# Kernel optimization log

Measured on AMD Instinct MI355X. Metric: run time of the kernel, lower is better.

The kernel has to match this reference:

```python
import jax, jax.numpy as jnp
from jax import lax
import numpy as np

K = 3          # kernel_size
PAD = 1        # K // 2
MAX_OFFSET = 0.1
EPS = 1e-8


def setup_inputs() -> dict:
    key = jax.random.key(0)
    k0, k1, k2 = jax.random.split(key, 3)
    B, C, H, W = 4, 64, 256, 256
    Cmid = C // 4
    x = jax.random.normal(k0, (B, C, H, W), jnp.float32)
    # offset_predictor: Conv2d(C+9, C//4, 3, pad=1) -> LeakyReLU(0.2) -> Conv2d(C//4, 2, 3, pad=1) -> Tanh
    w1 = jax.random.normal(k1, (Cmid, C + K * K, 3, 3), jnp.float32) * 0.05
    b1 = jnp.zeros((Cmid,), jnp.float32)
    w2 = jax.random.normal(k2, (2, Cmid, 3, 3), jnp.float32) * 0.05
    b2 = jnp.zeros((2,), jnp.float32)
    return {"x": x, "w1": w1, "b1": b1, "w2": w2, "b2": b2}


def _conv2d(x, w, b):
    # NCHW, OIHW, stride 1, pad 1 (SAME for 3x3)
    out = lax.conv_general_dilated(x, w, (1, 1), ((PAD, PAD), (PAD, PAD)),
                                   dimension_numbers=("NCHW", "OIHW", "NCHW"))
    return out + b[None, :, None, None]


def _local_cosine_similarity(x):
    # F.unfold with zero padding: neighbors[k] at spatial shift (di-1, dj-1), row-major k = di*K + dj
    B, C, H, W = x.shape
    xp = jnp.pad(x, ((0, 0), (0, 0), (PAD, PAD), (PAD, PAD)))
    neighbors = jnp.stack([xp[:, :, di:di + H, dj:dj + W]
                           for di in range(K) for dj in range(K)], axis=2)  # (B,C,9,H,W)
    center = x[:, :, None, :, :]                                            # (B,C,1,H,W)
    numerator = jnp.sum(neighbors * center, axis=1)                         # (B,9,H,W)
    center_norm = jnp.sqrt(jnp.sum(x * x, axis=1)) + EPS                    # (B,H,W)
    neighbor_norm = jnp.sqrt(jnp.sum(neighbors * neighbors, axis=1)) + EPS  # (B,9,H,W)
    return numerator / (center_norm[:, None] * neighbor_norm)               # (B,9,H,W)


def _grid_sample_border(x, grid):
    # bilinear, padding_mode='border', align_corners=True; grid: (B,H,W,2) with (gx,gy) in [-1,1]
    B, C, H, W = x.shape
    ix = (grid[..., 0] + 1.0) * 0.5 * (W - 1)
    iy = (grid[..., 1] + 1.0) * 0.5 * (H - 1)
    ix = jnp.clip(ix, 0.0, W - 1)
    iy = jnp.clip(iy, 0.0, H - 1)
    x0f = jnp.floor(ix); y0f = jnp.floor(iy)
    wx = ix - x0f; wy = iy - y0f
    x0 = x0f.astype(jnp.int32); y0 = y0f.astype(jnp.int32)
    x1 = jnp.minimum(x0 + 1, W - 1); y1 = jnp.minimum(y0 + 1, H - 1)

    def gather(img, yy, xx):  # img (C,H,W), yy/xx (H,W) -> (C,H,W)
        return img[:, yy, xx]

    g = jax.vmap(gather)
    v00 = g(x, y0, x0); v01 = g(x, y0, x1)
    v10 = g(x, y1, x0); v11 = g(x, y1, x1)
    wx = wx[:, None]; wy = wy[:, None]  # broadcast over channel dim
    return ((1 - wy) * ((1 - wx) * v00 + wx * v01)
            + wy * ((1 - wx) * v10 + wx * v11))


def reference(x, w1, b1, w2, b2):
    B, C, H, W = x.shape
    sim = _local_cosine_similarity(x)                       # (B,9,H,W)
    features = jnp.concatenate([x, sim], axis=1)            # (B,C+9,H,W)
    h = _conv2d(features, w1, b1)
    h = jnp.where(h >= 0, h, 0.2 * h)                       # LeakyReLU(0.2)
    offset = jnp.tanh(_conv2d(h, w2, b2)) * MAX_OFFSET      # (B,2,H,W)
    gy, gx = jnp.meshgrid(jnp.linspace(-1.0, 1.0, H),
                          jnp.linspace(-1.0, 1.0, W), indexing="ij")
    base_grid = jnp.stack([gx, gy], axis=-1)[None]          # (1,H,W,2)
    offset_grid = base_grid + jnp.transpose(offset, (0, 2, 3, 1))
    return _grid_sample_border(x, offset_grid)
```

## Files before the change

kernel.cpp:

```cpp
#include <hip/hip_runtime.h>
#include <math.h>

#define B 4
#define C 64
#define H 256
#define W 256
#define CMID 16
#define CIN 73
#define HW (H*W)
#define NW (CIN*9*CMID)
#define XS_STRIDE 260

__global__ void transpose_w1_kernel(const float* __restrict__ w1, float* __restrict__ wt) {
    int tid = blockIdx.x * blockDim.x + threadIdx.x;
    if (tid >= NW) return;
    int co = tid & (CMID - 1);
    int rest = tid >> 4;
    int ci = rest / 9;
    int k = rest - ci * 9;
    wt[tid] = w1[(co * CIN + ci) * 9 + k];
}

__device__ __forceinline__ void read_patch_lds(const float* __restrict__ xsbuf,
                                               int rl, int px, float v[3][4]) {
    const float* pb = xsbuf + rl * XS_STRIDE + px;
#pragma unroll
    for (int r = 0; r < 3; ++r) {
        float2 p0 = *(const float2*)(pb + r * XS_STRIDE);
        float2 p1 = *(const float2*)(pb + r * XS_STRIDE + 2);
        v[r][0] = p0.x; v[r][1] = p0.y; v[r][2] = p1.x; v[r][3] = p1.y;
    }
}

__global__ __launch_bounds__(256) void sim_kernel(const float* __restrict__ x,
                                                  float* __restrict__ sim) {
    __shared__ float xs[2][4 * XS_STRIDE];
    int bid = blockIdx.x;
    int b  = bid >> 7;
    int y0 = (bid & 127) << 1;
    int tid = threadIdx.x;
    int srow = tid >> 6;
    int sx4  = (tid & 63) << 2;
    int rl = tid >> 7;
    int px = (tid & 127) << 1;
    int y  = y0 + rl;

    int grow = y0 - 1 + srow;
    bool gvalid = (grow >= 0) && (grow < H);
    const float* gsrc = x + (size_t)b * C * HW + (size_t)grow * W + sx4;

    if (tid < 16) {
        int bu = tid >> 3, r = (tid >> 1) & 3, e = (tid & 1) ? 257 : 0;
        xs[bu][r * XS_STRIDE + e] = 0.f;
    }

    float dot0[9], dot1[9], nsq0[9], nsq1[9];
    float csq0 = 0.f, csq1 = 0.f;
#pragma unroll
    for (int i = 0; i < 9; ++i) { dot0[i] = dot1[i] = nsq0[i] = nsq1[i] = 0.f; }

    float4 r4 = make_float4(0.f, 0.f, 0.f, 0.f);
    if (gvalid) r4 = *(const float4*)gsrc;

    int cur = 0;
#pragma unroll 1
    for (int ci = 0; ci < C; ++ci) {
        float* dst = &xs[cur][srow * XS_STRIDE + 1 + sx4];
        dst[0] = r4.x; dst[1] = r4.y; dst[2] = r4.z; dst[3] = r4.w;
        __syncthreads();
        if (ci + 1 < C) {
            r4 = make_float4(0.f, 0.f, 0.f, 0.f);
            if (gvalid) r4 = *(const float4*)(gsrc + (size_t)(ci + 1) * HW);
        }
        float v[3][4];
        read_patch_lds(xs[cur], rl, px, v);
        float cv0 = v[1][1], cv1 = v[1][2];
        csq0 = fmaf(cv0, cv0, csq0);
        csq1 = fmaf(cv1, cv1, csq1);
#pragma unroll
        for (int kr = 0; kr < 3; ++kr)
#pragma unroll
            for (int kc = 0; kc < 3; ++kc) {
                int kk = kr * 3 + kc;
                if (kk == 4) continue;
                float n0 = v[kr][kc], n1 = v[kr][kc + 1];
                dot0[kk] = fmaf(cv0, n0, dot0[kk]);
                nsq0[kk] = fmaf(n0, n0, nsq0[kk]);
                dot1[kk] = fmaf(cv1, n1, dot1[kk]);
                nsq1[kk] = fmaf(n1, n1, nsq1[kk]);
            }
        cur ^= 1;
    }
    dot0[4] = csq0; nsq0[4] = csq0;
    dot1[4] = csq1; nsq1[4] = csq1;

    float cn0 = sqrtf(csq0) + 1e-8f;
    float cn1 = sqrtf(csq1) + 1e-8f;
    float* so = sim + (size_t)b * 9 * HW + (size_t)y * W + px;
#pragma unroll
    for (int kk = 0; kk < 9; ++kk) {
        float s0 = dot0[kk] / (cn0 * (sqrtf(nsq0[kk]) + 1e-8f));
        float s1 = dot1[kk] / (cn1 * (sqrtf(nsq1[kk]) + 1e-8f));
        *(float2*)(so + (size_t)kk * HW) = make_float2(s0, s1);
    }
}

__global__ __launch_bounds__(256) void conv1_kernel(const float* __restrict__ x,
                                                    const float* __restrict__ sim,
                                                    const float* __restrict__ wt,
                                                    const float* __restrict__ b1,
                                                    float* __restrict__ h) {
    __shared__ float lw[NW];
    __shared__ float xs[2][4 * XS_STRIDE];

    int tid = threadIdx.x;
    for (int j = tid; j < NW / 4; j += 256)
        ((float4*)lw)[j] = ((const float4*)wt)[j];

    int bid = blockIdx.x;
    int b  = bid >> 7;
    int y0 = (bid & 127) << 1;
    int srow = tid >> 6;
    int sx4  = (tid & 63) << 2;
    int rl = tid >> 7;
    int px = (tid & 127) << 1;
    int y  = y0 + rl;

    int grow = y0 - 1 + srow;
    bool gvalid = (grow >= 0) && (grow < H);
    const float* gx = x   + (size_t)b * C * HW + (size_t)grow * W + sx4;
    const float* gs = sim + (size_t)b * 9 * HW + (size_t)grow * W + sx4;

    if (tid < 16) {
        int bu = tid >> 3, r = (tid >> 1) & 3, e = (tid & 1) ? 257 : 0;
        xs[bu][r * XS_STRIDE + e] = 0.f;
    }

    float acc0[CMID], acc1[CMID];
#pragma unroll
    for (int co = 0; co < CMID; ++co) { acc0[co] = b1[co]; acc1[co] = b1[co]; }

    float4 r4 = make_float4(0.f, 0.f, 0.f, 0.f);
    if (gvalid) r4 = *(const float4*)gx;

    int cur = 0;
#pragma unroll 1
    for (int ci = 0; ci < CIN; ++ci) {
        float* dst = &xs[cur][srow * XS_STRIDE + 1 + sx4];
        dst[0] = r4.x; dst[1] = r4.y; dst[2] = r4.z; dst[3] = r4.w;
        __syncthreads();
        if (ci + 1 < CIN) {
            const float* src = (ci + 1 < C) ? (gx + (size_t)(ci + 1) * HW)
                                            : (gs + (size_t)(ci + 1 - C) * HW);
            r4 = make_float4(0.f, 0.f, 0.f, 0.f);
            if (gvalid) r4 = *(const float4*)src;
        }
        float v[3][4];
        read_patch_lds(xs[cur], rl, px, v);
        const float* wp = lw + ci * 144;
#pragma unroll
        for (int kr = 0; kr < 3; ++kr)
#pragma unroll
            for (int kc = 0; kc < 3; ++kc) {
                float a0 = v[kr][kc], a1 = v[kr][kc + 1];
                const float4* w4 = (const float4*)(wp + (kr * 3 + kc) * CMID);
#pragma unroll
                for (int q = 0; q < 4; ++q) {
                    float4 wv = w4[q];
                    acc0[4 * q + 0] = fmaf(a0, wv.x, acc0[4 * q + 0]);
                    acc0[4 * q + 1] = fmaf(a0, wv.y, acc0[4 * q + 1]);
                    acc0[4 * q + 2] = fmaf(a0, wv.z, acc0[4 * q + 2]);
                    acc0[4 * q + 3] = fmaf(a0, wv.w, acc0[4 * q + 3]);
                    acc1[4 * q + 0] = fmaf(a1, wv.x, acc1[4 * q + 0]);
                    acc1[4 * q + 1] = fmaf(a1, wv.y, acc1[4 * q + 1]);
                    acc1[4 * q + 2] = fmaf(a1, wv.z, acc1[4 * q + 2]);
                    acc1[4 * q + 3] = fmaf(a1, wv.w, acc1[4 * q + 3]);
                }
            }
        cur ^= 1;
    }

    float* ho = h + (size_t)b * CMID * HW + (size_t)y * W + px;
#pragma unroll
    for (int co = 0; co < CMID; ++co) {
        float v0 = acc0[co], v1 = acc1[co];
        v0 = v0 >= 0.f ? v0 : 0.2f * v0;
        v1 = v1 >= 0.f ? v1 : 0.2f * v1;
        *(float2*)(ho + (size_t)co * HW) = make_float2(v0, v1);
    }
}

__global__ __launch_bounds__(256) void offset_kernel(const float* __restrict__ h,
                                                     const float* __restrict__ w2,
                                                     const float* __restrict__ b2,
                                                     float2* __restrict__ off_buf) {
    __shared__ float lw2[CMID * 9 * 2];
    __shared__ float xs[2][4 * XS_STRIDE];

    int tid = threadIdx.x;
    for (int i = tid; i < CMID * 9 * 2; i += 256) {
        int co = i & 1;
        int rest = i >> 1;
        int ci = rest / 9;
        int kk = rest - ci * 9;
        lw2[i] = w2[(co * CMID + ci) * 9 + kk];
    }

    int bid = blockIdx.x;
    int b  = bid >> 7;
    int y0 = (bid & 127) << 1;
    int srow = tid >> 6;
    int sx4  = (tid & 63) << 2;
    int rl = tid >> 7;
    int px = (tid & 127) << 1;
    int y  = y0 + rl;

    int grow = y0 - 1 + srow;
    bool gvalid = (grow >= 0) && (grow < H);
    const float* gh = h + (size_t)b * CMID * HW + (size_t)grow * W + sx4;

    if (tid < 16) {
        int bu = tid >> 3, r = (tid >> 1) & 3, e = (tid & 1) ? 257 : 0;
        xs[bu][r * XS_STRIDE + e] = 0.f;
    }

    float s0x = b2[0], s0y = b2[1], s1x = b2[0], s1y = b2[1];

    float4 r4 = make_float4(0.f, 0.f, 0.f, 0.f);
    if (gvalid) r4 = *(const float4*)gh;

    int cur = 0;
#pragma unroll 1
    for (int ci = 0; ci < CMID; ++ci) {
        float* dst = &xs[cur][srow * XS_STRIDE + 1 + sx4];
        dst[0] = r4.x; dst[1] = r4.y; dst[2] = r4.z; dst[3] = r4.w;
        __syncthreads();
        if (ci + 1 < CMID) {
            r4 = make_float4(0.f, 0.f, 0.f, 0.f);
            if (gvalid) r4 = *(const float4*)(gh + (size_t)(ci + 1) * HW);
        }
        float v[3][4];
        read_patch_lds(xs[cur], rl, px, v);
#pragma unroll
        for (int kr = 0; kr < 3; ++kr)
#pragma unroll
            for (int kc = 0; kc < 3; ++kc) {
                float2 wv = *(const float2*)(lw2 + (ci * 9 + kr * 3 + kc) * 2);
                s0x = fmaf(v[kr][kc],     wv.x, s0x);
                s0y = fmaf(v[kr][kc],     wv.y, s0y);
                s1x = fmaf(v[kr][kc + 1], wv.x, s1x);
                s1y = fmaf(v[kr][kc + 1], wv.y, s1y);
            }
        cur ^= 1;
    }

    float ix0 = (float)px       + 0.1f * tanhf(s0x) * (0.5f * (float)(W - 1));
    float iy0 = (float)y        + 0.1f * tanhf(s0y) * (0.5f * (float)(H - 1));
    float ix1 = (float)(px + 1) + 0.1f * tanhf(s1x) * (0.5f * (float)(W - 1));
    float iy1 = (float)y        + 0.1f * tanhf(s1y) * (0.5f * (float)(H - 1));
    ix0 = fminf(fmaxf(ix0, 0.f), (float)(W - 1));
    iy0 = fminf(fmaxf(iy0, 0.f), (float)(H - 1));
    ix1 = fminf(fmaxf(ix1, 0.f), (float)(W - 1));
    iy1 = fminf(fmaxf(iy1, 0.f), (float)(H - 1));

    float4* op = (float4*)(off_buf + (size_t)b * HW + (size_t)y * W + px);
    *op = make_float4(ix0, iy0, ix1, iy1);
}

#define SROWS 35
__global__ __launch_bounds__(256) void sample_kernel(const float* __restrict__ x,
                                                     const float2* __restrict__ off_buf,
                                                     float* __restrict__ out) {
    __shared__ float xs[SROWS * 256];

    int bid = blockIdx.x;
    int sb = (bid & 7) * 16 + (bid >> 3);
    int b  = sb >> 5;
    int ty = sb & 31;
    int cg = blockIdx.y;
    int tid = threadIdx.x;

    int ybase = ty << 3;
    int lo = ybase - 13;

    int a00[8], a01[8], a10[8], a11[8];
    float wx[8], wy[8];
    const float2* ob2 = off_buf + (size_t)b * HW + (size_t)ybase * W + tid;
#pragma unroll
    for (int r = 0; r < 8; ++r) {
        float2 o = ob2[r * W];
        float xf = floorf(o.x), yf = floorf(o.y);
        wx[r] = o.x - xf; wy[r] = o.y - yf;
        int x0 = (int)xf, yy0 = (int)yf;
        int x1 = min(x0 + 1, W - 1), yy1 = min(yy0 + 1, H - 1);
        int r0 = (yy0 - lo) << 8, r1 = (yy1 - lo) << 8;
        a00[r] = r0 + x0; a01[r] = r0 + x1;
        a10[r] = r1 + x0; a11[r] = r1 + x1;
    }

    const float* xb = x + ((size_t)b * C + cg * 4) * HW;
    float* outb = out + ((size_t)b * C + cg * 4) * HW + (size_t)ybase * W + tid;

#pragma unroll 1
    for (int c = 0; c < 4; ++c) {
        __syncthreads();
        const float* src = xb + (size_t)c * HW;
        for (int j = tid; j < SROWS * 64; j += 256) {
            int row = j >> 6, x4 = (j & 63) << 2;
            int grw = min(max(lo + row, 0), H - 1);
            *(float4*)&xs[(row << 8) + x4] = *(const float4*)(src + (size_t)grw * W + x4);
        }
        __syncthreads();
        float* oc = outb + (size_t)c * HW;
#pragma unroll
        for (int r = 0; r < 8; ++r) {
            float v00 = xs[a00[r]], v01 = xs[a01[r]];
            float v10 = xs[a10[r]], v11 = xs[a11[r]];
            float top = fmaf(wx[r], v01 - v00, v00);
            float bot = fmaf(wx[r], v11 - v10, v10);
            oc[r * W] = fmaf(wy[r], bot - top, top);
        }
    }
}

extern "C" void kernel_launch(void* const* d_in, const int* in_sizes, int n_in,
                              void* d_out, int out_size, void* d_ws, size_t ws_size,
                              hipStream_t stream) {
    const float* x  = (const float*)d_in[0];
    const float* w1 = (const float*)d_in[1];
    const float* b1 = (const float*)d_in[2];
    const float* w2 = (const float*)d_in[3];
    const float* b2 = (const float*)d_in[4];
    float* out = (float*)d_out;

    float* ws  = (float*)d_ws;
    float* wt  = ws;
    float* sim = ws + 16384;
    float* h   = sim + (size_t)B * 9 * HW;
    float2* off_buf = (float2*)(h + (size_t)B * CMID * HW);

    transpose_w1_kernel<<<(NW + 255) / 256, 256, 0, stream>>>(w1, wt);

    sim_kernel<<<512, 256, 0, stream>>>(x, sim);
    conv1_kernel<<<512, 256, 0, stream>>>(x, sim, wt, b1, h);
    offset_kernel<<<512, 256, 0, stream>>>(h, w2, b2, off_buf);
    sample_kernel<<<dim3(128, 16), 256, 0, stream>>>(x, off_buf, out);
}
```

Measured before the change: 283.5 us.

## Read conv1 weights from global and stage two channels per barrier

The conv1 kernel no longer copies the roughly 42 KB transposed weight table into shared memory. It reads the weights straight from global memory with block-uniform addresses, which the compiler can turn into scalar constant-cache loads. The input channel loop now stages two channels per iteration in a double-buffered LDS tile, halving the number of barriers and prefetching two float4 rows ahead. This frees most of the LDS per block for higher occupancy and cuts synchronisation, at the risk of SGPR pressure or cache-miss latency on the weight loads.

New measurement: 262.9 us. -7.3%, faster.

```diff
diff --git a/kernel.cpp b/kernel.cpp
--- a/kernel.cpp
+++ b/kernel.cpp
@@ -105,18 +105,35 @@
     }
 }
 
+__device__ __forceinline__ void conv1_chan(const float* __restrict__ xsbuf,
+                                           int rl, int px,
+                                           const float* __restrict__ wp,
+                                           float acc0[CMID], float acc1[CMID]) {
+    float v[3][4];
+    read_patch_lds(xsbuf, rl, px, v);
+#pragma unroll
+    for (int kr = 0; kr < 3; ++kr)
+#pragma unroll
+        for (int kc = 0; kc < 3; ++kc) {
+            float a0 = v[kr][kc], a1 = v[kr][kc + 1];
+            const float* w = wp + (kr * 3 + kc) * CMID;
+#pragma unroll
+            for (int co = 0; co < CMID; ++co) {
+                float wv = w[co];
+                acc0[co] = fmaf(a0, wv, acc0[co]);
+                acc1[co] = fmaf(a1, wv, acc1[co]);
+            }
+        }
+}
+
 __global__ __launch_bounds__(256) void conv1_kernel(const float* __restrict__ x,
                                                     const float* __restrict__ sim,
                                                     const float* __restrict__ wt,
                                                     const float* __restrict__ b1,
                                                     float* __restrict__ h) {
-    __shared__ float lw[NW];
-    __shared__ float xs[2][4 * XS_STRIDE];
+    __shared__ float xs[2][2][4 * XS_STRIDE];
 
     int tid = threadIdx.x;
-    for (int j = tid; j < NW / 4; j += 256)
-        ((float4*)lw)[j] = ((const float4*)wt)[j];
-
     int bid = blockIdx.x;
     int b  = bid >> 7;
     int y0 = (bid & 127) << 1;
@@ -131,52 +148,45 @@
     const float* gx = x   + (size_t)b * C * HW + (size_t)grow * W + sx4;
     const float* gs = sim + (size_t)b * 9 * HW + (size_t)grow * W + sx4;
 
-    if (tid < 16) {
-        int bu = tid >> 3, r = (tid >> 1) & 3, e = (tid & 1) ? 257 : 0;
-        xs[bu][r * XS_STRIDE + e] = 0.f;
+    if (tid < 32) {
+        int bu = tid >> 4, ch = (tid >> 3) & 1, r = (tid >> 1) & 3;
+        int e = (tid & 1) ? 257 : 0;
+        xs[bu][ch][r * XS_STRIDE + e] = 0.f;
     }
 
     float acc0[CMID], acc1[CMID];
 #pragma unroll
     for (int co = 0; co < CMID; ++co) { acc0[co] = b1[co]; acc1[co] = b1[co]; }
 
-    float4 r4 = make_float4(0.f, 0.f, 0.f, 0.f);
-    if (gvalid) r4 = *(const float4*)gx;
+    float4 p0 = make_float4(0.f, 0.f, 0.f, 0.f), p1 = p0;
+    if (gvalid) {
+        p0 = *(const float4*)gx;
+        p1 = *(const float4*)(gx + HW);
+    }
 
     int cur = 0;
 #pragma unroll 1
-    for (int ci = 0; ci < CIN; ++ci) {
-        float* dst = &xs[cur][srow * XS_STRIDE + 1 + sx4];
-        dst[0] = r4.x; dst[1] = r4.y; dst[2] = r4.z; dst[3] = r4.w;
-        __syncthreads();
-        if (ci + 1 < CIN) {
-            const float* src = (ci + 1 < C) ? (gx + (size_t)(ci + 1) * HW)
-                                            : (gs + (size_t)(ci + 1 - C) * HW);
-            r4 = make_float4(0.f, 0.f, 0.f, 0.f);
-            if (gvalid) r4 = *(const float4*)src;
-        }
-        float v[3][4];
-        read_patch_lds(xs[cur], rl, px, v);
-        const float* wp = lw + ci * 144;
-#pragma unroll
-        for (int kr = 0; kr < 3; ++kr)
-#pragma unroll
-            for (int kc = 0; kc < 3; ++kc) {
-                float a0 = v[kr][kc], a1 = v[kr][kc + 1];
-                const float4* w4 = (const float4*)(wp + (kr * 3 + kc) * CMID);
-#pragma unroll
-                for (int q = 0; q < 4; ++q) {
-                    float4 wv = w4[q];
-                    acc0[4 * q + 0] = fmaf(a0, wv.x, acc0[4 * q + 0]);
-                    acc0[4 * q + 1] = fmaf(a0, wv.y, acc0[4 * q + 1]);
-                    acc0[4 * q + 2] = fmaf(a0, wv.z, acc0[4 * q + 2]);
-                    acc0[4 * q + 3] = fmaf(a0, wv.w, acc0[4 * q + 3]);
-                    acc1[4 * q + 0] = fmaf(a1, wv.x, acc1[4 * q + 0]);
-                    acc1[4 * q + 1] = fmaf(a1, wv.y, acc1[4 * q + 1]);
-                    acc1[4 * q + 2] = fmaf(a1, wv.z, acc1[4 * q + 2]);
-                    acc1[4 * q + 3] = fmaf(a1, wv.w, acc1[4 * q + 3]);
-                }
-            }
+    for (int cc = 0; cc < CIN; cc += 2) {
+        float* d0 = &xs[cur][0][srow * XS_STRIDE + 1 + sx4];
+        float* d1 = &xs[cur][1][srow * XS_STRIDE + 1 + sx4];
+        d0[0] = p0.x; d0[1] = p0.y; d0[2] = p0.z; d0[3] = p0.w;
+        d1[0] = p1.x; d1[1] = p1.y; d1[2] = p1.z; d1[3] = p1.w;
+        __syncthreads();
+
+        if (cc + 2 < CIN && gvalid) {
+            int ci = cc + 2;
+            p0 = (ci < C) ? *(const float4*)(gx + (size_t)ci * HW)
+                          : *(const float4*)(gs + (size_t)(ci - C) * HW);
+        }
+        if (cc + 3 < CIN && gvalid) {
+            int ci = cc + 3;
+            p1 = (ci < C) ? *(const float4*)(gx + (size_t)ci * HW)
+                          : *(const float4*)(gs + (size_t)(ci - C) * HW);
+        }
+
+        conv1_chan(xs[cur][0], rl, px, wt + cc * 144, acc0, acc1);
+        if (cc + 1 < CIN)
+            conv1_chan(xs[cur][1], rl, px, wt + (cc + 1) * 144, acc0, acc1);
         cur ^= 1;
     }
 
```
